# Performance work log

Measured on AMD Instinct MI355X. Metric: run time of the kernel, lower is better.

The kernel has to match this reference:

```python
import jax, jax.numpy as jnp
import numpy as np

D_MODEL = 1024
NHEAD = 16
HEAD_DIM = D_MODEL // NHEAD  # 64
THETA = 10000.0


def apply_rope(t):
    # t: [B, H, S, D]. Interleaved-pair RoPE (lucidrains rotary-embedding-torch
    # rotate_queries_or_keys), positions = arange(S), theta = 10000.
    B, H, S, D = t.shape
    inv_freq = 1.0 / (THETA ** (jnp.arange(0, D, 2, dtype=jnp.float32) / D))  # [D/2]
    ang = jnp.arange(S, dtype=jnp.float32)[:, None] * inv_freq               # [S, D/2]
    cos = jnp.cos(ang).astype(t.dtype)
    sin = jnp.sin(ang).astype(t.dtype)
    tp = t.reshape(B, H, S, D // 2, 2)
    x1, x2 = tp[..., 0], tp[..., 1]
    rot = jnp.stack([x1 * cos - x2 * sin, x1 * sin + x2 * cos], axis=-1)
    return rot.reshape(B, H, S, D)


def setup_inputs() -> dict:
    key = jax.random.key(0)
    k0, k1, k2, k3, k4 = jax.random.split(key, 5)
    B, Sx, Sc = 2, 2048, 2048
    sc = 0.02  # weight init scale
    return {
        "x": jax.random.normal(k0, (B, Sx, D_MODEL), jnp.float32),
        "context": jax.random.normal(k1, (B, Sc, D_MODEL), jnp.float32),
        "Wq": jax.random.normal(k2, (D_MODEL, D_MODEL), jnp.float32) * sc,
        "Wv": jax.random.normal(k3, (D_MODEL, D_MODEL), jnp.float32) * sc,
        "Wo": jax.random.normal(k4, (D_MODEL, D_MODEL), jnp.float32) * sc,
        "bo": jnp.zeros((D_MODEL,), jnp.float32),
        "x_pos": jnp.arange(B * Sx, dtype=jnp.int64).reshape(B, Sx) % Sx,
        "context_pos": jnp.arange(B * Sc, dtype=jnp.int64).reshape(B, Sc) % Sc,
    }


def reference(x, context, Wq, Wv, Wo, bo, x_pos, context_pos):
    # x_pos/context_pos are unused when both streams use the internal
    # RotaryEmbedding (is_imu1=is_imu2=True), matching the original forward.
    B, Sx, _ = x.shape
    Sc = context.shape[1]
    q = (x @ Wq.T).reshape(B, Sx, NHEAD, HEAD_DIM).transpose(0, 2, 1, 3)
    # NOTE: original code uses projq (not projk) for keys — replicated here.
    k = (context @ Wq.T).reshape(B, Sc, NHEAD, HEAD_DIM).transpose(0, 2, 1, 3)
    v = (context @ Wv.T).reshape(B, Sc, NHEAD, HEAD_DIM).transpose(0, 2, 1, 3)
    q = apply_rope(q)
    k = apply_rope(k)
    scale = 1.0 / jnp.sqrt(jnp.asarray(HEAD_DIM, q.dtype))
    attn = jax.nn.softmax(jnp.einsum("bhqd,bhkd->bhqk", q, k) * scale, axis=-1)
    out = jnp.einsum("bhqk,bhkd->bhqd", attn, v)            # [B,H,Sx,hd]
    out = out.transpose(0, 2, 1, 3).reshape(B, Sx, D_MODEL)  # [B,Sx,d_model]
    return out @ Wo.T + bo
```

## Files before the change

kernel.cpp:

```cpp
#include <hip/hip_runtime.h>
#include <cmath>


typedef __bf16 bf16x8 __attribute__((ext_vector_type(8)));
typedef __bf16 bf16x4 __attribute__((ext_vector_type(4)));
typedef float f32x4 __attribute__((ext_vector_type(4)));

#define MFMA(A, B, C) __builtin_amdgcn_mfma_f32_16x16x32_bf16(A, B, C, 0, 0, 0)
#define GLL16(g, l)                                                        \
  __builtin_amdgcn_global_load_lds(                                        \
      (const __attribute__((address_space(1))) unsigned int*)(g),          \
      (__attribute__((address_space(3))) unsigned int*)(l), 16, 0, 0)

__global__ __launch_bounds__(256) void cvt_all_kernel(
    const float* __restrict__ x, const float* __restrict__ ctx,
    const float* __restrict__ Wq, const float* __restrict__ Wv,
    const float* __restrict__ Wo, __bf16* __restrict__ xb, __bf16* __restrict__ cb,
    __bf16* __restrict__ Wqb, __bf16* __restrict__ Wvb, __bf16* __restrict__ Wob) {
  int base = blockIdx.x * 512 + threadIdx.x;
  const float* src;
  __bf16* dst;
  int off;
  if (base < 1048576) { src = x; dst = xb; off = 0; }
  else if (base < 2097152) { src = ctx; dst = cb; off = 1048576; }
  else if (base < 2359296) { src = Wq; dst = Wqb; off = 2097152; }
  else if (base < 2621440) { src = Wv; dst = Wvb; off = 2359296; }
  else { src = Wo; dst = Wob; off = 2621440; }
#pragma unroll
  for (int jj = 0; jj < 2; jj++) {
    int j = base - off + jj * 256;
    float4 f = ((const float4*)src)[j];
    bf16x4 o;
    o[0] = (__bf16)f.x; o[1] = (__bf16)f.y; o[2] = (__bf16)f.z; o[3] = (__bf16)f.w;
    ((bf16x4*)dst)[j] = o;
  }
}

__global__ __launch_bounds__(256) void gemm_proj(const __bf16* __restrict__ A0,
                                                 const __bf16* __restrict__ W0,
                                                 void* __restrict__ outQ,
                                                 void* __restrict__ outK,
                                                 void* __restrict__ outV) {
  const int tid = threadIdx.x;
  const int wave = tid >> 6, lane = tid & 63, quad = lane >> 4, l15 = lane & 15;
  const int mw = wave >> 1, nw = wave & 1;

  const int id = blockIdx.x;
  int m0, n0;
  const __bf16* A;
  const __bf16* W;
  bool vmode;
  if (id < 512) {
    const int xcd = id & 7, j = id >> 3;
    m0 = (xcd * 8 + (j & 7)) * 128;
    n0 = (j >> 3) * 128;
    A = A0;
    W = W0;
    vmode = false;
  } else {
    const int vid = id - 512;
    const int xcd = vid & 7, j = vid >> 3;
    m0 = (xcd * 4 + (j & 3)) * 128;
    n0 = (j >> 2) * 128;
    A = A0 + (size_t)4096 * 1024;
    W = W0 + (size_t)1024 * 1024;
    vmode = true;
  }

  __shared__ __attribute__((aligned(16))) __bf16 As[3][4096];
  __shared__ __attribute__((aligned(16))) __bf16 Ws[3][4096];

  int goff[2];
#pragma unroll
  for (int jj = 0; jj < 2; jj++) {
    const int s = jj * 256 + tid;
    const int row = s >> 2;
    const int kcg = (s & 3) ^ ((row >> 1) & 3);
    goff[jj] = row * 1024 + kcg * 8;
  }
  const __bf16* Ag = A + (size_t)m0 * 1024;
  const __bf16* Wg = W + (size_t)n0 * 1024;
  const int ldsoff0 = wave * 512;
  const int ldsoff1 = 2048 + wave * 512;

  const int sw = (l15 >> 1) & 3;
  int afoff[4], wfoff[4];
#pragma unroll
  for (int t = 0; t < 4; t++) {
    afoff[t] = (mw * 64 + t * 16 + l15) * 32 + (quad ^ sw) * 8;
    wfoff[t] = (nw * 64 + t * 16 + l15) * 32 + (quad ^ sw) * 8;
  }

  f32x4 acc[4][4] = {};

  auto stage = [&](int buf, int k0) {
    GLL16(Ag + goff[0] + k0, &As[buf][ldsoff0]);
    GLL16(Ag + goff[1] + k0, &As[buf][ldsoff1]);
    GLL16(Wg + goff[0] + k0, &Ws[buf][ldsoff0]);
    GLL16(Wg + goff[1] + k0, &Ws[buf][ldsoff1]);
  };
  auto compute = [&](int buf) {
    bf16x8 af[4], wf[4];
#pragma unroll
    for (int t = 0; t < 4; t++) af[t] = *(const bf16x8*)&As[buf][afoff[t]];
#pragma unroll
    for (int t = 0; t < 4; t++) wf[t] = *(const bf16x8*)&Ws[buf][wfoff[t]];
#pragma unroll
    for (int mt = 0; mt < 4; mt++)
#pragma unroll
      for (int nt = 0; nt < 4; nt++) acc[mt][nt] = MFMA(af[mt], wf[nt], acc[mt][nt]);
  };

  stage(0, 0);
  stage(1, 32);
  int buf = 0;
  for (int c = 0; c < 32; c++) {
    __syncthreads();
    if (c + 2 < 32) {
      int nb = buf + 2;
      if (nb >= 3) nb -= 3;
      stage(nb, (c + 2) * 32);
    }
    compute(buf);
    buf = (buf == 2) ? 0 : buf + 1;
  }

  if (!vmode) {
    const int isK = (m0 >= 4096);
    __bf16* O = (__bf16*)(isK ? outK : outQ);
    const float qsc = isK ? 1.0f : 0.18033688f;
    const int mb = m0 & 4095;
#pragma unroll
    for (int nt = 0; nt < 4; nt++) {
      const int n = n0 + nw * 64 + nt * 16 + l15;
      const int h = n >> 6, d = n & 63, p = d >> 1;
      const float invf_rev =
          __builtin_amdgcn_exp2f(-((float)p * 0.41524101f + 2.6514961f));
#pragma unroll
      for (int mt = 0; mt < 4; mt++) {
#pragma unroll
        for (int r = 0; r < 4; r++) {
          const int row = mb + mw * 64 + mt * 16 + quad * 4 + r;
          const int s = row & 2047, b = row >> 11;
          float v = acc[mt][nt][r];
          float pv = __shfl_xor(v, 1, 64);
          float fr = __builtin_amdgcn_fractf((float)s * invf_rev);
          float sn = __builtin_amdgcn_sinf(fr);
          float cs = __builtin_amdgcn_cosf(fr);
          float res = (lane & 1) ? (pv * sn + v * cs) : (v * cs - pv * sn);
          O[((size_t)(b * 16 + h) * 2048 + s) * 64 + d] = (__bf16)(res * qsc);
        }
      }
    }
  } else {
    __bf16* O = (__bf16*)outV;
#pragma unroll
    for (int nt = 0; nt < 4; nt++) {
      const int n = n0 + nw * 64 + nt * 16 + l15;
      const int h = n >> 6, d = n & 63;
#pragma unroll
      for (int mt = 0; mt < 4; mt++) {
        const int rowb = m0 + mw * 64 + mt * 16 + quad * 4;
        const int s = rowb & 2047, b = rowb >> 11;
        bf16x4 o;
#pragma unroll
        for (int r = 0; r < 4; r++) o[r] = (__bf16)acc[mt][nt][r];
        *(bf16x4*)(O + ((size_t)(b * 16 + h) * 64 + d) * 2048 + s) = o;
      }
    }
  }
}

__global__ __launch_bounds__(256) void gemm_out(const __bf16* __restrict__ A,
                                                const __bf16* __restrict__ W,
                                                float* __restrict__ O,
                                                const float* __restrict__ bias) {
  const int tid = threadIdx.x;
  const int wave = tid >> 6, lane = tid & 63, quad = lane >> 4, l15 = lane & 15;
  const int mw = wave >> 1, nw = wave & 1;
  const int id = blockIdx.x;
  const int xcd = id & 7, j = id >> 3;
  const int m0 = (xcd * 4 + (j & 3)) * 128;
  const int n0 = (j >> 2) * 64;

  __shared__ __attribute__((aligned(16))) __bf16 As[3][4096];
  __shared__ __attribute__((aligned(16))) __bf16 Ws[3][2048];

  int goff[2];
#pragma unroll
  for (int jj = 0; jj < 2; jj++) {
    const int s = jj * 256 + tid;
    const int row = s >> 2;
    const int kcg = (s & 3) ^ ((row >> 1) & 3);
    goff[jj] = row * 1024 + kcg * 8;
  }
  const int wrow = tid >> 2;
  const int wkcg = (tid & 3) ^ ((wrow >> 1) & 3);
  const int goffw = wrow * 1024 + wkcg * 8;

  const __bf16* Ag = A + (size_t)m0 * 1024;
  const __bf16* Wg = W + (size_t)n0 * 1024;
  const int ldsoff0 = wave * 512;
  const int ldsoff1 = 2048 + wave * 512;

  const int sw = (l15 >> 1) & 3;
  int afoff[4], wfoff[2];
#pragma unroll
  for (int t = 0; t < 4; t++)
    afoff[t] = (mw * 64 + t * 16 + l15) * 32 + (quad ^ sw) * 8;
#pragma unroll
  for (int t = 0; t < 2; t++)
    wfoff[t] = (nw * 32 + t * 16 + l15) * 32 + (quad ^ sw) * 8;

  f32x4 acc[4][2] = {};

  auto stage = [&](int buf, int k0) {
    GLL16(Ag + goff[0] + k0, &As[buf][ldsoff0]);
    GLL16(Ag + goff[1] + k0, &As[buf][ldsoff1]);
    GLL16(Wg + goffw + k0, &Ws[buf][ldsoff0]);
  };
  auto compute = [&](int buf) {
    bf16x8 af[4], wf[2];
#pragma unroll
    for (int t = 0; t < 4; t++) af[t] = *(const bf16x8*)&As[buf][afoff[t]];
#pragma unroll
    for (int t = 0; t < 2; t++) wf[t] = *(const bf16x8*)&Ws[buf][wfoff[t]];
#pragma unroll
    for (int mt = 0; mt < 4; mt++)
#pragma unroll
      for (int nt = 0; nt < 2; nt++) acc[mt][nt] = MFMA(af[mt], wf[nt], acc[mt][nt]);
  };

  stage(0, 0);
  stage(1, 32);
  int buf = 0;
  for (int c = 0; c < 32; c++) {
    __syncthreads();
    if (c + 2 < 32) {
      int nb = buf + 2;
      if (nb >= 3) nb -= 3;
      stage(nb, (c + 2) * 32);
    }
    compute(buf);
    buf = (buf == 2) ? 0 : buf + 1;
  }

#pragma unroll
  for (int nt = 0; nt < 2; nt++) {
    const int n = n0 + nw * 32 + nt * 16 + l15;
    const float bv = bias[n];
#pragma unroll
    for (int mt = 0; mt < 4; mt++) {
#pragma unroll
      for (int r = 0; r < 4; r++) {
        const int row = m0 + mw * 64 + mt * 16 + quad * 4 + r;
        O[(size_t)row * 1024 + n] = acc[mt][nt][r] + bv;
      }
    }
  }
}

__global__ __launch_bounds__(512) void attn_kernel(const __bf16* __restrict__ Q,
                                                   const __bf16* __restrict__ K,
                                                   const __bf16* __restrict__ Vt,
                                                   __bf16* __restrict__ Aout) {
  const int tid = threadIdx.x;
  const int wave = tid >> 6, lane = tid & 63, quad = lane >> 4, l15 = lane & 15;
  const int id = blockIdx.x;
  const int j = id >> 3;
  const int bh = ((id & 7) << 2) | (j & 3);
  const int q0 = (j >> 2) << 7;

  const __bf16* Qb = Q + (size_t)bh * (2048 * 64);
  const __bf16* Kb = K + (size_t)bh * (2048 * 64);
  const __bf16* Vb = Vt + (size_t)bh * (64 * 2048);

  __shared__ __attribute__((aligned(16))) __bf16 Kbuf[4][4096];
  __shared__ __attribute__((aligned(16))) __bf16 Vbuf[4][4096];
  __shared__ __attribute__((aligned(16))) __bf16 Plds[8][8][16][8];

  bf16x8 qf[2];
  {
    const __bf16* qp = Qb + (size_t)(q0 + wave * 16 + l15) * 64 + quad * 8;
    qf[0] = *(const bf16x8*)qp;
    qf[1] = *(const bf16x8*)(qp + 32);
  }

  const int s0 = wave * 64 + lane;
  const int r0 = s0 >> 3, c0 = (s0 & 7) ^ (r0 & 7);
  const __bf16* kg0 = Kb + r0 * 64 + c0 * 8;
  const __bf16* vg0 = Vb + r0 * 2048 + c0 * 8;
  const int klds = wave * 512;

  const int offF0 = l15 * 64 + ((quad ^ (l15 & 7)) * 8);
  const int offF1 = l15 * 64 + (((4 + quad) ^ (l15 & 7)) * 8);

  f32x4 rs4 = {};
  f32x4 oT[4] = {};

  auto stage = [&](int buf, int kt) {
    GLL16(kg0 + kt * 64, &Kbuf[buf][klds]);
    GLL16(vg0 + kt, &Vbuf[buf][klds]);
  };
  auto compute = [&](int buf) {
    f32x4 sT[4];
#pragma unroll
    for (int nt = 0; nt < 4; nt++) {
      bf16x8 kf0 = *(const bf16x8*)&Kbuf[buf][nt * 1024 + offF0];
      bf16x8 kf1 = *(const bf16x8*)&Kbuf[buf][nt * 1024 + offF1];
      f32x4 z = {};
      z = MFMA(kf0, qf[0], z);
      sT[nt] = MFMA(kf1, qf[1], z);
    }
#pragma unroll
    for (int nt = 0; nt < 4; nt++) {
      bf16x4 pb;
      f32x4 pe;
#pragma unroll
      for (int r = 0; r < 4; r++) {
        pe[r] = __builtin_amdgcn_exp2f(sT[nt][r]);
        pb[r] = (__bf16)pe[r];
      }
      rs4 += pe;
      const int chunk = nt * 2 + (quad >> 1);
      *(bf16x4*)&Plds[wave][chunk][l15 ^ ((chunk & 3) << 1)][(quad & 1) * 4] = pb;
    }
    bf16x8 pf0 = *(const bf16x8*)&Plds[wave][quad][l15 ^ (quad << 1)][0];
    bf16x8 pf1 = *(const bf16x8*)&Plds[wave][4 + quad][l15 ^ (quad << 1)][0];
#pragma unroll
    for (int nt = 0; nt < 4; nt++) {
      bf16x8 vf0 = *(const bf16x8*)&Vbuf[buf][nt * 1024 + offF0];
      bf16x8 vf1 = *(const bf16x8*)&Vbuf[buf][nt * 1024 + offF1];
      oT[nt] = MFMA(vf0, pf0, oT[nt]);
      oT[nt] = MFMA(vf1, pf1, oT[nt]);
    }
  };

  stage(0, 0);
  stage(1, 64);
  for (int kt = 0; kt < 2048; kt += 128) {
    const int p = (kt >> 7) & 1;
    __syncthreads();
    if (kt + 128 < 2048) {
      stage(2 * (p ^ 1), kt + 128);
      stage(2 * (p ^ 1) + 1, kt + 192);
    }
    compute(2 * p);
    compute(2 * p + 1);
  }

  const int b = bh >> 4, h = bh & 15;
  float l = (rs4[0] + rs4[1]) + (rs4[2] + rs4[3]);
  l += __shfl_xor(l, 16, 64);
  l += __shfl_xor(l, 32, 64);
  const float inv = 1.f / l;
  const int q = q0 + wave * 16 + l15;
#pragma unroll
  for (int nt = 0; nt < 4; nt++) {
    bf16x4 o;
#pragma unroll
    for (int r = 0; r < 4; r++) o[r] = (__bf16)(oT[nt][r] * inv);
    *(bf16x4*)&Aout[((size_t)(b * 2048 + q)) * 1024 + h * 64 + nt * 16 + quad * 4] = o;
  }
}

extern "C" void kernel_launch(void* const* d_in, const int* in_sizes, int n_in,
                              void* d_out, int out_size, void* d_ws, size_t ws_size,
                              hipStream_t stream) {
  const float* x   = (const float*)d_in[0];
  const float* ctx = (const float*)d_in[1];
  const float* Wq  = (const float*)d_in[2];
  const float* Wv  = (const float*)d_in[3];
  const float* Wo  = (const float*)d_in[4];
  const float* bo  = (const float*)d_in[5];

  char* ws = (char*)d_ws;
  const size_t MB = 1024 * 1024;
  __bf16* xb   = (__bf16*)(ws + 0 * MB);
  __bf16* cb   = (__bf16*)(ws + 8 * MB);
  __bf16* Wqb  = (__bf16*)(ws + 16 * MB);
  __bf16* Wvb  = (__bf16*)(ws + 18 * MB);
  __bf16* Wob  = (__bf16*)(ws + 20 * MB);
  __bf16* qh   = (__bf16*)(ws + 22 * MB);
  __bf16* kh   = (__bf16*)(ws + 30 * MB);
  __bf16* vt   = (__bf16*)(ws + 38 * MB);
  __bf16* attn = xb;

  cvt_all_kernel<<<5632, 256, 0, stream>>>(x, ctx, Wq, Wv, Wo, xb, cb, Wqb, Wvb, Wob);

  gemm_proj<<<768, 256, 0, stream>>>(xb, Wqb, (void*)qh, (void*)kh, (void*)vt);

  attn_kernel<<<512, 512, 0, stream>>>(qh, kh, vt, attn);

  gemm_out<<<512, 256, 0, stream>>>(attn, Wob, (float*)d_out, bo);
}
```

Before: 203.9 us.

## Use 32x32 MFMA in attention with register-resident P and split-K waves

Rewrites the attention inner loop to use 32x32x16 bf16 MFMAs. Waves are split into query groups and key halves, and P is packed into bf16 in registers with cvt_pk and permlane32_swap instead of a round trip through LDS. Partial outputs and row sums from the two key-half waves are combined through LDS at the end. The goal is to cut LDS traffic and instruction count per tile, at the cost of an extra reduction phase and non-vectorized scalar bf16 output stores.

After: 201.7 us. Within noise of the previous version (-1.1%).

```diff
diff --git a/kernel.cpp b/kernel.cpp
--- a/kernel.cpp
+++ b/kernel.cpp
@@ -5,8 +5,11 @@
 typedef __bf16 bf16x8 __attribute__((ext_vector_type(8)));
 typedef __bf16 bf16x4 __attribute__((ext_vector_type(4)));
 typedef float f32x4 __attribute__((ext_vector_type(4)));
+typedef float f32x16 __attribute__((ext_vector_type(16)));
+typedef unsigned u32x4v __attribute__((ext_vector_type(4)));
 
 #define MFMA(A, B, C) __builtin_amdgcn_mfma_f32_16x16x32_bf16(A, B, C, 0, 0, 0)
+#define MFMA32(A, B, C) __builtin_amdgcn_mfma_f32_32x32x16_bf16(A, B, C, 0, 0, 0)
 #define GLL16(g, l)                                                        \
   __builtin_amdgcn_global_load_lds(                                        \
       (const __attribute__((address_space(1))) unsigned int*)(g),          \
@@ -260,12 +263,14 @@
   }
 }
 
-__global__ __launch_bounds__(512) void attn_kernel(const __bf16* __restrict__ Q,
-                                                   const __bf16* __restrict__ K,
-                                                   const __bf16* __restrict__ Vt,
-                                                   __bf16* __restrict__ Aout) {
+__global__ __launch_bounds__(512, 4) void attn_kernel(const __bf16* __restrict__ Q,
+                                                      const __bf16* __restrict__ K,
+                                                      const __bf16* __restrict__ Vt,
+                                                      __bf16* __restrict__ Aout) {
   const int tid = threadIdx.x;
-  const int wave = tid >> 6, lane = tid & 63, quad = lane >> 4, l15 = lane & 15;
+  const int wave = tid >> 6, lane = tid & 63;
+  const int l31 = lane & 31, hi = lane >> 5;
+  const int qg = wave >> 1, kg = wave & 1;
   const int id = blockIdx.x;
   const int j = id >> 3;
   const int bh = ((id & 7) << 2) | (j & 3);
@@ -277,63 +282,76 @@
 
   __shared__ __attribute__((aligned(16))) __bf16 Kbuf[4][4096];
   __shared__ __attribute__((aligned(16))) __bf16 Vbuf[4][4096];
-  __shared__ __attribute__((aligned(16))) __bf16 Plds[8][8][16][8];
-
-  bf16x8 qf[2];
+
+  bf16x8 qf[4];
   {
-    const __bf16* qp = Qb + (size_t)(q0 + wave * 16 + l15) * 64 + quad * 8;
-    qf[0] = *(const bf16x8*)qp;
-    qf[1] = *(const bf16x8*)(qp + 32);
+    const __bf16* qp = Qb + (size_t)(q0 + qg * 32 + l31) * 64 + hi * 8;
+#pragma unroll
+    for (int i = 0; i < 4; i++) qf[i] = *(const bf16x8*)(qp + i * 16);
   }
 
   const int s0 = wave * 64 + lane;
   const int r0 = s0 >> 3, c0 = (s0 & 7) ^ (r0 & 7);
-  const __bf16* kg0 = Kb + r0 * 64 + c0 * 8;
-  const __bf16* vg0 = Vb + r0 * 2048 + c0 * 8;
+  const __bf16* kgp = Kb + r0 * 64 + c0 * 8;
+  const __bf16* vgp = Vb + r0 * 2048 + c0 * 8;
   const int klds = wave * 512;
 
-  const int offF0 = l15 * 64 + ((quad ^ (l15 & 7)) * 8);
-  const int offF1 = l15 * 64 + (((4 + quad) ^ (l15 & 7)) * 8);
+  int koff[4];
+  {
+    const int rk = kg * 32 + l31;
+#pragma unroll
+    for (int i = 0; i < 4; i++) koff[i] = rk * 64 + (((2 * i + hi) ^ (rk & 7)) * 8);
+  }
+  int voff[2][2];
+#pragma unroll
+  for (int dt = 0; dt < 2; dt++) {
+    const int rv = dt * 32 + l31;
+#pragma unroll
+    for (int ks = 0; ks < 2; ks++)
+      voff[dt][ks] = rv * 64 + (((kg * 4 + ks * 2 + hi) ^ (rv & 7)) * 8);
+  }
 
   f32x4 rs4 = {};
-  f32x4 oT[4] = {};
+  f32x16 oacc[2] = {};
 
   auto stage = [&](int buf, int kt) {
-    GLL16(kg0 + kt * 64, &Kbuf[buf][klds]);
-    GLL16(vg0 + kt, &Vbuf[buf][klds]);
-  };
+    GLL16(kgp + kt * 64, &Kbuf[buf][klds]);
+    GLL16(vgp + kt, &Vbuf[buf][klds]);
+  };
+
   auto compute = [&](int buf) {
-    f32x4 sT[4];
-#pragma unroll
-    for (int nt = 0; nt < 4; nt++) {
-      bf16x8 kf0 = *(const bf16x8*)&Kbuf[buf][nt * 1024 + offF0];
-      bf16x8 kf1 = *(const bf16x8*)&Kbuf[buf][nt * 1024 + offF1];
-      f32x4 z = {};
-      z = MFMA(kf0, qf[0], z);
-      sT[nt] = MFMA(kf1, qf[1], z);
-    }
-#pragma unroll
-    for (int nt = 0; nt < 4; nt++) {
-      bf16x4 pb;
-      f32x4 pe;
-#pragma unroll
-      for (int r = 0; r < 4; r++) {
-        pe[r] = __builtin_amdgcn_exp2f(sT[nt][r]);
-        pb[r] = (__bf16)pe[r];
+    f32x16 s = {};
+#pragma unroll
+    for (int i = 0; i < 4; i++) {
+      bf16x8 kf = *(const bf16x8*)&Kbuf[buf][koff[i]];
+      s = MFMA32(kf, qf[i], s);
+    }
+    float pe[16];
+#pragma unroll
+    for (int r = 0; r < 16; r++) pe[r] = __builtin_amdgcn_exp2f(s[r]);
+#pragma unroll
+    for (int r = 0; r < 16; r++) rs4[r & 3] += pe[r];
+    bf16x8 pa[2];
+#pragma unroll
+    for (int sl = 0; sl < 2; sl++) {
+      unsigned wa, wb, wc, wd;
+      asm("v_cvt_pk_bf16_f32 %0, %1, %2" : "=v"(wa) : "v"(pe[8 * sl + 0]), "v"(pe[8 * sl + 1]));
+      asm("v_cvt_pk_bf16_f32 %0, %1, %2" : "=v"(wb) : "v"(pe[8 * sl + 4]), "v"(pe[8 * sl + 5]));
+      asm("v_cvt_pk_bf16_f32 %0, %1, %2" : "=v"(wc) : "v"(pe[8 * sl + 2]), "v"(pe[8 * sl + 3]));
+      asm("v_cvt_pk_bf16_f32 %0, %1, %2" : "=v"(wd) : "v"(pe[8 * sl + 6]), "v"(pe[8 * sl + 7]));
+      asm("v_permlane32_swap_b32 %0, %1" : "+v"(wa), "+v"(wb));
+      asm("v_permlane32_swap_b32 %0, %1" : "+v"(wc), "+v"(wd));
+      u32x4v t;
+      t[0] = wa; t[1] = wc; t[2] = wb; t[3] = wd;
+      pa[sl] = __builtin_bit_cast(bf16x8, t);
+    }
+#pragma unroll
+    for (int dt = 0; dt < 2; dt++)
+#pragma unroll
+      for (int ks = 0; ks < 2; ks++) {
+        bf16x8 vf = *(const bf16x8*)&Vbuf[buf][voff[dt][ks]];
+        oacc[dt] = MFMA32(pa[ks], vf, oacc[dt]);
       }
-      rs4 += pe;
-      const int chunk = nt * 2 + (quad >> 1);
-      *(bf16x4*)&Plds[wave][chunk][l15 ^ ((chunk & 3) << 1)][(quad & 1) * 4] = pb;
-    }
-    bf16x8 pf0 = *(const bf16x8*)&Plds[wave][quad][l15 ^ (quad << 1)][0];
-    bf16x8 pf1 = *(const bf16x8*)&Plds[wave][4 + quad][l15 ^ (quad << 1)][0];
-#pragma unroll
-    for (int nt = 0; nt < 4; nt++) {
-      bf16x8 vf0 = *(const bf16x8*)&Vbuf[buf][nt * 1024 + offF0];
-      bf16x8 vf1 = *(const bf16x8*)&Vbuf[buf][nt * 1024 + offF1];
-      oT[nt] = MFMA(vf0, pf0, oT[nt]);
-      oT[nt] = MFMA(vf1, pf1, oT[nt]);
-    }
   };
 
   stage(0, 0);
@@ -349,18 +367,37 @@
     compute(2 * p + 1);
   }
 
-  const int b = bh >> 4, h = bh & 15;
-  float l = (rs4[0] + rs4[1]) + (rs4[2] + rs4[3]);
-  l += __shfl_xor(l, 16, 64);
-  l += __shfl_xor(l, 32, 64);
-  const float inv = 1.f / l;
-  const int q = q0 + wave * 16 + l15;
-#pragma unroll
-  for (int nt = 0; nt < 4; nt++) {
-    bf16x4 o;
-#pragma unroll
-    for (int r = 0; r < 4; r++) o[r] = (__bf16)(oT[nt][r] * inv);
-    *(bf16x4*)&Aout[((size_t)(b * 2048 + q)) * 1024 + h * 64 + nt * 16 + quad * 4] = o;
+  __syncthreads();
+  float* Ored = (float*)&Kbuf[0][0];
+  float* Lred = (float*)&Vbuf[0][0];
+
+  float lw = (rs4[0] + rs4[1]) + (rs4[2] + rs4[3]);
+  lw += __shfl_xor(lw, 32, 64);
+  Lred[wave * 64 + lane] = lw;
+  if (kg == 1) {
+#pragma unroll
+    for (int dt = 0; dt < 2; dt++)
+#pragma unroll
+      for (int r = 0; r < 16; r++)
+        Ored[(qg * 32 + dt * 16 + r) * 64 + lane] = oacc[dt][r];
+  }
+  __syncthreads();
+  if (kg == 0) {
+    const int b = bh >> 4, h = bh & 15;
+#pragma unroll
+    for (int r = 0; r < 16; r++) {
+      const int qrow = (r & 3) + 8 * (r >> 2) + 4 * hi;
+      const float lt =
+          Lred[(qg * 2) * 64 + qrow] + Lred[(qg * 2 + 1) * 64 + qrow];
+      const float inv = 1.f / lt;
+      const int qAbs = q0 + qg * 32 + qrow;
+#pragma unroll
+      for (int dt = 0; dt < 2; dt++) {
+        const float o = oacc[dt][r] + Ored[(qg * 32 + dt * 16 + r) * 64 + lane];
+        Aout[((size_t)(b * 2048 + qAbs)) * 1024 + h * 64 + dt * 32 + l31] =
+            (__bf16)(o * inv);
+      }
+    }
   }
 }
 
```
